# Kernel tuning notes

Hardware: AMD Instinct MI355X
Metric: run time of the kernel (lower is better)

The kernel has to match this reference:

```python
import jax, jax.numpy as jnp
import numpy as np
from jax import lax


def _b_mask(out_c, in_c, kh, kw):
    # MaskedConv2d mask_type='B' for a 1xK kernel: zero strictly right-of-center taps
    m = np.ones((out_c, in_c, kh, kw), dtype=np.float32)
    m[:, :, kh // 2:, kw // 2 + 1:] = 0
    m[:, :, kh // 2 + 1:, :] = 0
    return jnp.asarray(m)


def _conv(x, w, b):
    # NCHW 'same' conv, stride 1
    y = lax.conv_general_dilated(x, w, (1, 1), 'SAME',
                                 dimension_numbers=('NCHW', 'OIHW', 'NCHW'))
    return y + b[None, :, None, None]


def setup_inputs() -> dict:
    key = jax.random.key(0)
    ks = jax.random.split(key, 7)
    B, C_in, H, W = 32, 3, 64, 64
    HC = 128
    return {
        'x': jax.random.normal(ks[0], (B, C_in, H, W), jnp.float32),
        'W_is': jax.random.normal(ks[1], (4 * HC, C_in, 1, 3), jnp.float32) * 0.1,
        'b_is': jax.random.normal(ks[2], (4 * HC,), jnp.float32) * 0.1,
        'W_ss': jax.random.normal(ks[3], (4 * HC, HC, 1, 3), jnp.float32) * 0.1,
        'b_ss': jax.random.normal(ks[4], (4 * HC,), jnp.float32) * 0.1,
        'h0': jax.random.normal(ks[5], (1, HC, 1, W), jnp.float32) * 0.05,
        'c0': jax.random.normal(ks[6], (1, HC, 1, W), jnp.float32) * 0.05,
    }


def reference(x, W_is, b_is, W_ss, b_ss, h0, c0):
    B, _, H, W = x.shape
    HC = h0.shape[1]
    W_is_m = W_is * _b_mask(*W_is.shape)
    W_ss_m = W_ss * _b_mask(*W_ss.shape)

    # input-to-state projection for all rows at once: [B, 4*HC, H, W]
    x_proj = _conv(x, W_is_m, b_is)
    x_rows = jnp.moveaxis(x_proj, 2, 0)[:, :, :, None, :]  # [H, B, 4HC, 1, W]

    h_init = jnp.broadcast_to(h0, (B, HC, 1, W))
    c_init = jnp.broadcast_to(c0, (B, HC, 1, W))

    def step(carry, row_x):
        h_prev, c_prev = carry
        gates = jax.nn.sigmoid(row_x + _conv(h_prev, W_ss_m, b_ss))
        o, f, i, g = jnp.split(gates, 4, axis=1)
        c = f * c_prev + i * g
        h = o * jnp.tanh(c)
        return (h, c), h

    _, hs = lax.scan(step, (h_init, c_init), x_rows)  # hs: [H, B, HC, 1, W]
    hidden = jnp.moveaxis(hs[:, :, :, 0, :], 0, 2)  # [B, HC, H, W]
    return hidden
```

## Files before the change

### kernel.cpp

```cpp
#include <hip/hip_runtime.h>
#include <hip/hip_bf16.h>

typedef unsigned short u16;
typedef unsigned int u32;
typedef unsigned long long u64;
typedef short bf16x8 __attribute__((ext_vector_type(8)));
typedef float f32x4  __attribute__((ext_vector_type(4)));


__device__ __forceinline__ u16 f2b(float f) {
    return __builtin_bit_cast(u16, __float2bfloat16(f));
}
__device__ __forceinline__ float sigm(float x) {
    return __builtin_amdgcn_rcpf(1.0f + __expf(-x));
}
__device__ __forceinline__ float tanh_fast(float x) {
    return 1.0f - 2.0f * __builtin_amdgcn_rcpf(__expf(2.0f * x) + 1.0f);
}

#define LINE(kt, lane) (((kt) * 64 + (lane)) * 16)
#define BUFBYTES (9 * 64 * 16)

__global__ __launch_bounds__(512, 2) void rowlstm_mfma5(
    const float* __restrict__ x,   const float* __restrict__ Wis,
    const float* __restrict__ bis, const float* __restrict__ Wss,
    const float* __restrict__ bss, const float* __restrict__ h0,
    const float* __restrict__ c0,  float* __restrict__ out,
    u32* flags, char* halo)
{
    __shared__ __align__(16) char lds_buf[2 * BUFBYTES];
    __shared__ u16  lds_x[3 * 64 * 17];
    __shared__ float lds_bias[512];

    const int tid  = threadIdx.x;
    const int s    = blockIdx.x;
    const int b    = blockIdx.y;
    const int wid  = tid >> 6;
    const int lane = tid & 63;
    const int q    = lane >> 4;
    const int n    = lane & 15;
    const int wbase = s * 16;

    u32* flg_my = flags + ((size_t)b * 4 + s) * 8;
    u32* flg_up = flags + ((size_t)b * 4 + (s > 0 ? s - 1 : 0)) * 8;
    char* hs_my = halo + (((size_t)b * 4 + s) * 64) * 256;
    char* hs_up = halo + (((size_t)b * 4 + (s > 0 ? s - 1 : 0)) * 64) * 256;

    for (int i = tid; i < 1152; i += 512)
        *(uint4*)(lds_buf + i * 16) = make_uint4(0, 0, 0, 0);
    __syncthreads();

    lds_bias[tid] = bis[tid] + bss[tid];

    for (int i = tid; i < 3264; i += 512) {
        int cch = i / 1088, rem = i % 1088;
        int r = rem / 17, wl1 = rem % 17;
        int gw = wbase + wl1 - 1;
        lds_x[i] = (gw < 0) ? (u16)0
                 : f2b(x[(((size_t)b * 3 + cch) * 64 + r) * 64 + gw]);
    }

    bf16x8 afr[4][9];
    {
        #pragma unroll
        for (int g = 0; g < 4; ++g) {
            int oc = g * 128 + wid * 16 + n;
            #pragma unroll
            for (int kt = 0; kt < 8; ++kt) {
                bf16x8 a;
                #pragma unroll
                for (int jj = 0; jj < 4; ++jj) {
                    int ic = kt * 16 + q * 4 + jj;
                    float2 wp = *(const float2*)&Wss[(size_t)(oc * 128 + ic) * 3];
                    a[jj]     = (short)f2b(wp.y);
                    a[4 + jj] = (short)f2b(wp.x);
                }
                afr[g][kt] = a;
            }
            bf16x8 ax = {0, 0, 0, 0, 0, 0, 0, 0};
            if (q == 0) {
                #pragma unroll
                for (int cch = 0; cch < 3; ++cch) {
                    float2 wp = *(const float2*)&Wis[(size_t)(oc * 3 + cch) * 3];
                    ax[cch]     = (short)f2b(wp.y);
                    ax[4 + cch] = (short)f2b(wp.x);
                }
            }
            afr[g][8] = ax;
        }
    }

    float cst[4];
    {
        u16 hw[4];
        #pragma unroll
        for (int reg = 0; reg < 4; ++reg) {
            int hc = wid * 16 + q * 4 + reg;
            int wg = wbase + n;
            cst[reg] = c0[hc * 64 + wg];
            hw[reg] = f2b(h0[hc * 64 + wg]);
        }
        u64 d01 = (u64)((u32)hw[0] | ((u32)hw[1] << 16))
                | ((u64)((u32)hw[2] | ((u32)hw[3] << 16)) << 32);
        *(u64*)(lds_buf + LINE(wid, lane)) = d01;
        int wl = n + 1;
        if (wl < 16)
            *(u64*)(lds_buf + LINE(wid, q * 16 + wl) + 8) = d01;
    }
    if (s > 0 && tid < 32) {
        int ic0 = tid * 4;
        u64 v = (u64)((u32)f2b(h0[(ic0 + 0) * 64 + wbase - 1]) | ((u32)f2b(h0[(ic0 + 1) * 64 + wbase - 1]) << 16))
              | ((u64)((u32)f2b(h0[(ic0 + 2) * 64 + wbase - 1]) | ((u32)f2b(h0[(ic0 + 3) * 64 + wbase - 1]) << 16)) << 32);
        *(u64*)(lds_buf + LINE(tid >> 2, (tid & 3) * 16) + 8) = v;
    }
    if (tid < 16) {
        int nn = tid;
        u32 d0 = (u32)lds_x[0 * 1088 + 0 * 17 + nn + 1] | ((u32)lds_x[1 * 1088 + 0 * 17 + nn + 1] << 16);
        u32 d1 = (u32)lds_x[2 * 1088 + 0 * 17 + nn + 1];
        u32 d2 = (u32)lds_x[0 * 1088 + 0 * 17 + nn]     | ((u32)lds_x[1 * 1088 + 0 * 17 + nn] << 16);
        u32 d3 = (u32)lds_x[2 * 1088 + 0 * 17 + nn];
        *(uint4*)(lds_buf + LINE(8, nn)) = make_uint4(d0, d1, d2, d3);
    }
    __syncthreads();

    f32x4 bias_r[4];
    #pragma unroll
    for (int g = 0; g < 4; ++g) {
        int oc = g * 128 + wid * 16 + q * 4;
        bias_r[g][0] = lds_bias[oc + 0];
        bias_r[g][1] = lds_bias[oc + 1];
        bias_r[g][2] = lds_bias[oc + 2];
        bias_r[g][3] = lds_bias[oc + 3];
    }

    u32 flag_seen = 0;

    for (int r = 0; r < 64; ++r) {
        char* rbuf = lds_buf + (r & 1) * BUFBYTES;
        char* wbuf = lds_buf + ((r & 1) ^ 1) * BUFBYTES;

        u64 hv = 0; bool have = false;
        if (s > 0 && r < 63 && tid < 32) {
            u32 fs = flag_seen;
            while (fs <= (u32)r) {
                fs = __hip_atomic_load(&flg_up[tid >> 2], __ATOMIC_RELAXED,
                                       __HIP_MEMORY_SCOPE_AGENT);
                if (fs <= (u32)r) __builtin_amdgcn_s_sleep(1);
            }
            hv = __hip_atomic_load((u64*)(hs_up + (size_t)r * 256 + tid * 8),
                                   __ATOMIC_RELAXED, __HIP_MEMORY_SCOPE_AGENT);
            flag_seen = __hip_atomic_load(&flg_up[tid >> 2], __ATOMIC_RELAXED,
                                          __HIP_MEMORY_SCOPE_AGENT);
            have = true;
        }

        if (r < 63 && tid >= 64 && tid < 80) {
            int nn = tid - 64, r1 = r + 1;
            u32 d0 = (u32)lds_x[0 * 1088 + r1 * 17 + nn + 1] | ((u32)lds_x[1 * 1088 + r1 * 17 + nn + 1] << 16);
            u32 d1 = (u32)lds_x[2 * 1088 + r1 * 17 + nn + 1];
            u32 d2 = (u32)lds_x[0 * 1088 + r1 * 17 + nn]     | ((u32)lds_x[1 * 1088 + r1 * 17 + nn] << 16);
            u32 d3 = (u32)lds_x[2 * 1088 + r1 * 17 + nn];
            *(uint4*)(wbuf + LINE(8, nn)) = make_uint4(d0, d1, d2, d3);
        }

        f32x4 acc[4];
        acc[0] = bias_r[0]; acc[1] = bias_r[1];
        acc[2] = bias_r[2]; acc[3] = bias_r[3];
        #pragma unroll
        for (int kt = 0; kt < 9; ++kt) {
            bf16x8 bv = *(const bf16x8*)(rbuf + LINE(kt, lane));
            acc[0] = __builtin_amdgcn_mfma_f32_16x16x32_bf16(afr[0][kt], bv, acc[0], 0, 0, 0);
            acc[1] = __builtin_amdgcn_mfma_f32_16x16x32_bf16(afr[1][kt], bv, acc[1], 0, 0, 0);
            acc[2] = __builtin_amdgcn_mfma_f32_16x16x32_bf16(afr[2][kt], bv, acc[2], 0, 0, 0);
            acc[3] = __builtin_amdgcn_mfma_f32_16x16x32_bf16(afr[3][kt], bv, acc[3], 0, 0, 0);
        }

        float hval[4]; u16 hw[4];
        #pragma unroll
        for (int reg = 0; reg < 4; ++reg) {
            float o  = sigm(acc[0][reg]);
            float f  = sigm(acc[1][reg]);
            float ii = sigm(acc[2][reg]);
            float gg = sigm(acc[3][reg]);
            float cn = f * cst[reg] + ii * gg;
            cst[reg] = cn;
            float h = o * tanh_fast(cn);
            hval[reg] = h;
            hw[reg] = f2b(h);
        }

        if (s < 3 && r > 0 && lane == 15) {
            asm volatile("s_waitcnt vmcnt(0)" ::: "memory");
            __hip_atomic_store(&flg_my[wid], (u32)r,
                               __ATOMIC_RELAXED, __HIP_MEMORY_SCOPE_AGENT);
        }

        u64 d01 = (u64)((u32)hw[0] | ((u32)hw[1] << 16))
                | ((u64)((u32)hw[2] | ((u32)hw[3] << 16)) << 32);
        *(u64*)(wbuf + LINE(wid, lane)) = d01;
        int wl = n + 1;
        if (wl < 16)
            *(u64*)(wbuf + LINE(wid, q * 16 + wl) + 8) = d01;
        else if (s < 3 && r < 63)
            __hip_atomic_store((u64*)(hs_my + (size_t)r * 256 + (wid * 4 + q) * 8),
                               d01, __ATOMIC_RELAXED, __HIP_MEMORY_SCOPE_AGENT);

        #pragma unroll
        for (int reg = 0; reg < 4; ++reg) {
            int hc = wid * 16 + q * 4 + reg;
            out[(((size_t)(b * 128 + hc)) * 64 + r) * 64 + wbase + n] = hval[reg];
        }

        if (have)
            *(u64*)(wbuf + LINE(tid >> 2, (tid & 3) * 16) + 8) = hv;

        __syncthreads();
    }
}

extern "C" void kernel_launch(void* const* d_in, const int* in_sizes, int n_in,
                              void* d_out, int out_size, void* d_ws, size_t ws_size,
                              hipStream_t stream)
{
    const float* x   = (const float*)d_in[0];
    const float* Wis = (const float*)d_in[1];
    const float* bis = (const float*)d_in[2];
    const float* Wss = (const float*)d_in[3];
    const float* bss = (const float*)d_in[4];
    const float* h0  = (const float*)d_in[5];
    const float* c0  = (const float*)d_in[6];
    float* out = (float*)d_out;

    hipMemsetAsync(d_ws, 0, 4096, stream);
    rowlstm_mfma5<<<dim3(4, 32), 512, 0, stream>>>(
        x, Wis, bis, Wss, bss, h0, c0, out,
        (u32*)d_ws, (char*)d_ws + 4096);
}
```

Measured before the change: 208.4 us.

## Centralize halo export in one wave with single flag per block

```diff
diff --git a/kernel.cpp b/kernel.cpp
--- a/kernel.cpp
+++ b/kernel.cpp
@@ -21,7 +21,7 @@
 #define LINE(kt, lane) (((kt) * 64 + (lane)) * 16)
 #define BUFBYTES (9 * 64 * 16)
 
-__global__ __launch_bounds__(512, 2) void rowlstm_mfma5(
+__global__ __launch_bounds__(512, 2) void rowlstm_mfma6(
     const float* __restrict__ x,   const float* __restrict__ Wis,
     const float* __restrict__ bis, const float* __restrict__ Wss,
     const float* __restrict__ bss, const float* __restrict__ h0,
@@ -139,17 +139,30 @@
         char* rbuf = lds_buf + (r & 1) * BUFBYTES;
         char* wbuf = lds_buf + ((r & 1) ^ 1) * BUFBYTES;
 
+        if (s < 3 && wid == 7 && lane < 32) {
+            if (r >= 2 && lane == 0) {
+                asm volatile("s_waitcnt vmcnt(0)" ::: "memory");
+                __hip_atomic_store(&flg_my[0], (u32)(r - 1),
+                                   __ATOMIC_RELAXED, __HIP_MEMORY_SCOPE_AGENT);
+            }
+            if (r >= 1) {
+                u64 ev = *(const u64*)(rbuf + LINE(lane >> 2, (lane & 3) * 16 + 15));
+                __hip_atomic_store((u64*)(hs_my + (size_t)(r - 1) * 256 + lane * 8),
+                                   ev, __ATOMIC_RELAXED, __HIP_MEMORY_SCOPE_AGENT);
+            }
+        }
+
         u64 hv = 0; bool have = false;
         if (s > 0 && r < 63 && tid < 32) {
             u32 fs = flag_seen;
             while (fs <= (u32)r) {
-                fs = __hip_atomic_load(&flg_up[tid >> 2], __ATOMIC_RELAXED,
+                fs = __hip_atomic_load(&flg_up[0], __ATOMIC_RELAXED,
                                        __HIP_MEMORY_SCOPE_AGENT);
                 if (fs <= (u32)r) __builtin_amdgcn_s_sleep(1);
             }
             hv = __hip_atomic_load((u64*)(hs_up + (size_t)r * 256 + tid * 8),
                                    __ATOMIC_RELAXED, __HIP_MEMORY_SCOPE_AGENT);
-            flag_seen = __hip_atomic_load(&flg_up[tid >> 2], __ATOMIC_RELAXED,
+            flag_seen = __hip_atomic_load(&flg_up[0], __ATOMIC_RELAXED,
                                           __HIP_MEMORY_SCOPE_AGENT);
             have = true;
         }
@@ -189,21 +202,12 @@
             hw[reg] = f2b(h);
         }
 
-        if (s < 3 && r > 0 && lane == 15) {
-            asm volatile("s_waitcnt vmcnt(0)" ::: "memory");
-            __hip_atomic_store(&flg_my[wid], (u32)r,
-                               __ATOMIC_RELAXED, __HIP_MEMORY_SCOPE_AGENT);
-        }
-
         u64 d01 = (u64)((u32)hw[0] | ((u32)hw[1] << 16))
                 | ((u64)((u32)hw[2] | ((u32)hw[3] << 16)) << 32);
         *(u64*)(wbuf + LINE(wid, lane)) = d01;
         int wl = n + 1;
         if (wl < 16)
             *(u64*)(wbuf + LINE(wid, q * 16 + wl) + 8) = d01;
-        else if (s < 3 && r < 63)
-            __hip_atomic_store((u64*)(hs_my + (size_t)r * 256 + (wid * 4 + q) * 8),
-                               d01, __ATOMIC_RELAXED, __HIP_MEMORY_SCOPE_AGENT);
 
         #pragma unroll
         for (int reg = 0; reg < 4; ++reg) {
@@ -214,7 +218,15 @@
         if (have)
             *(u64*)(wbuf + LINE(tid >> 2, (tid & 3) * 16) + 8) = hv;
 
-        __syncthreads();
+        __builtin_amdgcn_sched_barrier(0);
+        asm volatile("s_waitcnt lgkmcnt(0)\n\ts_barrier" ::: "memory");
+        __builtin_amdgcn_sched_barrier(0);
+    }
+
+    if (s < 3 && tid == 448) {
+        asm volatile("s_waitcnt vmcnt(0)" ::: "memory");
+        __hip_atomic_store(&flg_my[0], 63u,
+                           __ATOMIC_RELAXED, __HIP_MEMORY_SCOPE_AGENT);
     }
 }
 
@@ -232,7 +244,7 @@
     float* out = (float*)d_out;
 
     hipMemsetAsync(d_ws, 0, 4096, stream);
-    rowlstm_mfma5<<<dim3(4, 32), 512, 0, stream>>>(
+    rowlstm_mfma6<<<dim3(4, 32), 512, 0, stream>>>(
         x, Wis, bis, Wss, bss, h0, c0, out,
         (u32*)d_ws, (char*)d_ws + 4096);
 }
```

Result: no change. 204.7 us (-1.8%).

## Replace flag-based halo handshake with self-validating inverted payload polling

Applied to the files above, without the earlier changes.

```diff
diff --git a/kernel.cpp b/kernel.cpp
--- a/kernel.cpp
+++ b/kernel.cpp
@@ -21,12 +21,12 @@
 #define LINE(kt, lane) (((kt) * 64 + (lane)) * 16)
 #define BUFBYTES (9 * 64 * 16)
 
-__global__ __launch_bounds__(512, 2) void rowlstm_mfma5(
+__global__ __launch_bounds__(512, 2) void rowlstm_mfma8(
     const float* __restrict__ x,   const float* __restrict__ Wis,
     const float* __restrict__ bis, const float* __restrict__ Wss,
     const float* __restrict__ bss, const float* __restrict__ h0,
     const float* __restrict__ c0,  float* __restrict__ out,
-    u32* flags, char* halo)
+    char* halo)
 {
     __shared__ __align__(16) char lds_buf[2 * BUFBYTES];
     __shared__ u16  lds_x[3 * 64 * 17];
@@ -41,10 +41,8 @@
     const int n    = lane & 15;
     const int wbase = s * 16;
 
-    u32* flg_my = flags + ((size_t)b * 4 + s) * 8;
-    u32* flg_up = flags + ((size_t)b * 4 + (s > 0 ? s - 1 : 0)) * 8;
-    char* hs_my = halo + (((size_t)b * 4 + s) * 64) * 256;
-    char* hs_up = halo + (((size_t)b * 4 + (s > 0 ? s - 1 : 0)) * 64) * 256;
+    char* hs_my = halo + ((size_t)(b * 4 + s) * 64) * 256;
+    char* hs_up = halo + ((size_t)(b * 4 + (s > 0 ? s - 1 : 0)) * 64) * 256;
 
     for (int i = tid; i < 1152; i += 512)
         *(uint4*)(lds_buf + i * 16) = make_uint4(0, 0, 0, 0);
@@ -133,26 +131,19 @@
         bias_r[g][3] = lds_bias[oc + 3];
     }
 
-    u32 flag_seen = 0;
+    u64 hv = 0, hn = 0;
+    const bool is_cons = (s > 0) && (tid < 32);
+    if (is_cons)
+        hv = __hip_atomic_load((const u64*)(hs_up + (size_t)tid * 8),
+                               __ATOMIC_RELAXED, __HIP_MEMORY_SCOPE_AGENT);
 
     for (int r = 0; r < 64; ++r) {
         char* rbuf = lds_buf + (r & 1) * BUFBYTES;
         char* wbuf = lds_buf + ((r & 1) ^ 1) * BUFBYTES;
 
-        u64 hv = 0; bool have = false;
-        if (s > 0 && r < 63 && tid < 32) {
-            u32 fs = flag_seen;
-            while (fs <= (u32)r) {
-                fs = __hip_atomic_load(&flg_up[tid >> 2], __ATOMIC_RELAXED,
-                                       __HIP_MEMORY_SCOPE_AGENT);
-                if (fs <= (u32)r) __builtin_amdgcn_s_sleep(1);
-            }
-            hv = __hip_atomic_load((u64*)(hs_up + (size_t)r * 256 + tid * 8),
+        if (is_cons && r < 62)
+            hn = __hip_atomic_load((const u64*)(hs_up + (size_t)(r + 1) * 256 + tid * 8),
                                    __ATOMIC_RELAXED, __HIP_MEMORY_SCOPE_AGENT);
-            flag_seen = __hip_atomic_load(&flg_up[tid >> 2], __ATOMIC_RELAXED,
-                                          __HIP_MEMORY_SCOPE_AGENT);
-            have = true;
-        }
 
         if (r < 63 && tid >= 64 && tid < 80) {
             int nn = tid - 64, r1 = r + 1;
@@ -189,21 +180,16 @@
             hw[reg] = f2b(h);
         }
 
-        if (s < 3 && r > 0 && lane == 15) {
-            asm volatile("s_waitcnt vmcnt(0)" ::: "memory");
-            __hip_atomic_store(&flg_my[wid], (u32)r,
-                               __ATOMIC_RELAXED, __HIP_MEMORY_SCOPE_AGENT);
-        }
-
         u64 d01 = (u64)((u32)hw[0] | ((u32)hw[1] << 16))
                 | ((u64)((u32)hw[2] | ((u32)hw[3] << 16)) << 32);
         *(u64*)(wbuf + LINE(wid, lane)) = d01;
         int wl = n + 1;
-        if (wl < 16)
+        if (wl < 16) {
             *(u64*)(wbuf + LINE(wid, q * 16 + wl) + 8) = d01;
-        else if (s < 3 && r < 63)
+        } else if (s < 3 && r < 63) {
             __hip_atomic_store((u64*)(hs_my + (size_t)r * 256 + (wid * 4 + q) * 8),
-                               d01, __ATOMIC_RELAXED, __HIP_MEMORY_SCOPE_AGENT);
+                               ~d01, __ATOMIC_RELAXED, __HIP_MEMORY_SCOPE_AGENT);
+        }
 
         #pragma unroll
         for (int reg = 0; reg < 4; ++reg) {
@@ -211,10 +197,19 @@
             out[(((size_t)(b * 128 + hc)) * 64 + r) * 64 + wbase + n] = hval[reg];
         }
 
-        if (have)
-            *(u64*)(wbuf + LINE(tid >> 2, (tid & 3) * 16) + 8) = hv;
-
-        __syncthreads();
+        if (is_cons && r < 63) {
+            while (hv == 0) {
+                __builtin_amdgcn_s_sleep(1);
+                hv = __hip_atomic_load((const u64*)(hs_up + (size_t)r * 256 + tid * 8),
+                                       __ATOMIC_RELAXED, __HIP_MEMORY_SCOPE_AGENT);
+            }
+            *(u64*)(wbuf + LINE(tid >> 2, (tid & 3) * 16) + 8) = ~hv;
+            hv = hn;
+        }
+
+        __builtin_amdgcn_sched_barrier(0);
+        asm volatile("s_waitcnt lgkmcnt(0)\n\ts_barrier" ::: "memory");
+        __builtin_amdgcn_sched_barrier(0);
     }
 }
 
@@ -231,8 +226,7 @@
     const float* c0  = (const float*)d_in[6];
     float* out = (float*)d_out;
 
-    hipMemsetAsync(d_ws, 0, 4096, stream);
-    rowlstm_mfma5<<<dim3(4, 32), 512, 0, stream>>>(
-        x, Wis, bis, Wss, bss, h0, c0, out,
-        (u32*)d_ws, (char*)d_ws + 4096);
-}
+    hipMemsetAsync(d_ws, 0, (size_t)32 * 4 * 64 * 256, stream);
+    rowlstm_mfma8<<<dim3(4, 32), 512, 0, stream>>>(
+        x, Wis, bis, Wss, bss, h0, c0, out, (char*)d_ws);
+}
```

After: 205.5 us. Within noise of the previous version (-1.4%).
